# Kernel optimization log

Hardware: AMD Instinct MI355X
Metric: run time of the kernel (lower is better)

The kernel has to match this reference:

```python
import jax, jax.numpy as jnp
import numpy as np

B, S, D, H = 2, 2048, 1024, 16
HD = D // H
MAX_SEQ_LEN = 2048
ROPE_BASE = 10000.0


def _rope(x, pos):
    # x: [B,S,H,HD], pos: [B,S] int positions (already abs+clamped)
    inv_freq = 1.0 / (ROPE_BASE ** (jnp.arange(0, HD, 2, dtype=jnp.float32) / HD))  # [HD/2]
    freqs = pos.astype(jnp.float32)[..., None] * inv_freq  # [B,S,HD/2]
    cos = jnp.cos(freqs)[:, :, None, :]  # [B,S,1,HD/2]
    sin = jnp.sin(freqs)[:, :, None, :]
    x1, x2 = x[..., : HD // 2], x[..., HD // 2 :]
    return jnp.concatenate([x1 * cos - x2 * sin, x2 * cos + x1 * sin], axis=-1)


def setup_inputs() -> dict:
    key = jax.random.key(0)
    ks = jax.random.split(key, 8)
    std = 1.0 / np.sqrt(D)
    x = jax.random.normal(ks[0], (B, S, D), dtype=jnp.float32)
    Wq = jax.random.normal(ks[1], (D, D), dtype=jnp.float32) * std
    Wk = jax.random.normal(ks[2], (D, D), dtype=jnp.float32) * std
    Wv = jax.random.normal(ks[3], (D, D), dtype=jnp.float32) * std
    Wo = jax.random.normal(ks[4], (D, D), dtype=jnp.float32) * std
    bq = jnp.zeros((D,), jnp.float32)
    bk = jnp.zeros((D,), jnp.float32)
    bv = jnp.zeros((D,), jnp.float32)
    bo = jnp.zeros((D,), jnp.float32)
    decay_rate = jnp.float32(0.1)
    # causal mask [B,S,S]
    mask = jnp.broadcast_to(jnp.tril(jnp.ones((S, S), jnp.int32)), (B, S, S))
    # sorted day offsets per batch (monotone time axis)
    days_offset = jnp.sort(jax.random.randint(ks[5], (B, S), 0, MAX_SEQ_LEN), axis=-1).astype(jnp.int32)
    return {"x": x, "Wq": Wq, "bq": bq, "Wk": Wk, "bk": bk, "Wv": Wv, "bv": bv,
            "Wo": Wo, "bo": bo, "decay_rate": decay_rate, "mask": mask, "days_offset": days_offset}


def reference(x, Wq, bq, Wk, bk, Wv, bv, Wo, bo, decay_rate, mask, days_offset):
    b, s, _ = x.shape
    q = (x @ Wq.T + bq).reshape(b, s, H, HD)
    k = (x @ Wk.T + bk).reshape(b, s, H, HD)
    v = (x @ Wv.T + bv).reshape(b, s, H, HD)
    pos = jnp.clip(jnp.abs(days_offset), 0, MAX_SEQ_LEN - 1)
    q = _rope(q, pos)
    k = _rope(k, pos)
    scores = jnp.einsum("bqhd,bkhd->bhqk", q, k) / np.sqrt(HD).astype(np.float32)
    dist = jnp.abs(days_offset[:, :, None] - days_offset[:, None, :]).astype(jnp.float32)  # [B,S,S]
    decay = jnp.exp(-decay_rate * dist)
    scores = scores * decay[:, None, :, :]
    scores = jnp.where(mask[:, None, :, :] == 0, -jnp.inf, scores)
    attn = jax.nn.softmax(scores, axis=-1)
    out = jnp.einsum("bhqk,bkhd->bqhd", attn, v).reshape(b, s, D)
    return out @ Wo.T + bo
```

## Files before the change

kernel.cpp:

```cpp
#include <hip/hip_runtime.h>
#include <hip/hip_bf16.h>


typedef unsigned short u16;
typedef short bf16x8 __attribute__((ext_vector_type(8)));
typedef float f32x4 __attribute__((ext_vector_type(4)));

__device__ __forceinline__ u16 f2bf(float f) {
    unsigned u = __builtin_bit_cast(unsigned, f);
    u += 0x7fffu + ((u >> 16) & 1u);
    return (u16)(u >> 16);
}
__device__ __forceinline__ float bf2f(u16 h) {
    unsigned u = ((unsigned)h) << 16;
    return __builtin_bit_cast(float, u);
}

__global__ __launch_bounds__(256) void convert_all_k(const float* __restrict__ x,
                                                     const float* __restrict__ wq,
                                                     const float* __restrict__ wk,
                                                     const float* __restrict__ wv,
                                                     const float* __restrict__ wo_,
                                                     u16* __restrict__ xb,
                                                     u16* __restrict__ wqkv,
                                                     u16* __restrict__ wob) {
    int i = (blockIdx.x * 256 + threadIdx.x) * 4;
    const float* src;
    u16* dst;
    int off;
    if (i < 4194304) {
        src = x; dst = xb; off = i;
    } else if (i < 5242880) {
        src = wq; dst = wqkv; off = i - 4194304;
    } else if (i < 6291456) {
        src = wk; dst = wqkv + 1048576; off = i - 5242880;
    } else if (i < 7340032) {
        src = wv; dst = wqkv + 2097152; off = i - 6291456;
    } else {
        src = wo_; dst = wob; off = i - 7340032;
    }
    float4 v = *(const float4*)(src + off);
    uint2 o;
    o.x = (unsigned)f2bf(v.x) | ((unsigned)f2bf(v.y) << 16);
    o.y = (unsigned)f2bf(v.z) | ((unsigned)f2bf(v.w) << 16);
    *(uint2*)(dst + off) = o;
}

template <int EPI>
__global__ __launch_bounds__(256) void gemm_bt(const u16* __restrict__ A,
                                               const u16* __restrict__ Bw,
                                               const float* __restrict__ bias0,
                                               const float* __restrict__ bias1,
                                               const float* __restrict__ bias2,
                                               const int* __restrict__ days,
                                               u16* __restrict__ outB,
                                               float* __restrict__ outF,
                                               int M, int N, int K) {
    __shared__ __align__(16) u16 As[2][4096];
    __shared__ __align__(16) u16 Bs[2][4096];
    const int tid = threadIdx.x;
    const int lane = tid & 63;
    const int w = tid >> 6;
    const int wr = w >> 1, wc = w & 1;
    const int lr = lane & 15, lg = lane >> 4;
    const int nbn = N >> 7;
    const int m0 = (blockIdx.x / nbn) << 7;
    const int n0 = (blockIdx.x % nbn) << 7;

    f32x4 acc[4][4] = {};

    const u16* aptr[2];
    const u16* bptr[2];
    int ldsoff[2];
#pragma unroll
    for (int i = 0; i < 2; ++i) {
        int c = (w * 2 + i) * 64 + lane;
        int row = c >> 2, kc = (c & 3) << 3;
        aptr[i] = A + (size_t)(m0 + row) * K + kc;
        bptr[i] = Bw + (size_t)(n0 + row) * K + kc;
        ldsoff[i] = (w * 2 + i) * 512;
    }

#define GSTAGE(K0, BUF)                                                                \
    do {                                                                               \
        _Pragma("unroll") for (int i = 0; i < 2; ++i) {                                \
            __builtin_amdgcn_global_load_lds(                                          \
                (const __attribute__((address_space(1))) void*)(aptr[i] + (K0)),       \
                (__attribute__((address_space(3))) void*)(&As[BUF][ldsoff[i]]), 16, 0, \
                0);                                                                    \
            __builtin_amdgcn_global_load_lds(                                          \
                (const __attribute__((address_space(1))) void*)(bptr[i] + (K0)),       \
                (__attribute__((address_space(3))) void*)(&Bs[BUF][ldsoff[i]]), 16, 0, \
                0);                                                                    \
        }                                                                              \
    } while (0)

    const int nks = K >> 5;
    GSTAGE(0, 0);
    for (int ks = 0; ks < nks; ++ks) {
        const int cur = ks & 1;
        if (ks + 1 < nks) {
            GSTAGE((ks + 1) * 32, cur ^ 1);
            asm volatile("s_waitcnt vmcnt(4)" ::: "memory");
        } else {
            asm volatile("s_waitcnt vmcnt(0)" ::: "memory");
        }
        __builtin_amdgcn_s_barrier();
        bf16x8 af[4], bfr[4];
#pragma unroll
        for (int i = 0; i < 4; ++i)
            af[i] = *(const bf16x8*)(&As[cur][(wr * 64 + i * 16 + lr) * 32 + lg * 8]);
#pragma unroll
        for (int j = 0; j < 4; ++j)
            bfr[j] = *(const bf16x8*)(&Bs[cur][(wc * 64 + j * 16 + lr) * 32 + lg * 8]);
#pragma unroll
        for (int i = 0; i < 4; ++i)
#pragma unroll
            for (int j = 0; j < 4; ++j)
                acc[i][j] = __builtin_amdgcn_mfma_f32_16x16x32_bf16(af[i], bfr[j],
                                                                    acc[i][j], 0, 0, 0);
        __builtin_amdgcn_s_barrier();
    }
#undef GSTAGE

    auto bsel = [&](int ng) -> float {
        if (EPI != 0) return bias0[ng];
        return (ng < 1024) ? bias0[ng] : (ng < 2048) ? bias1[ng - 1024] : bias2[ng - 2048];
    };

    if (EPI == 0 && (n0 + wc * 64) < 2048) {
        const float C1 = -0.41524101186091903f;
        const float inv0 = exp2f((float)lr * C1);
        const float inv1 = exp2f((float)(16 + lr) * C1);
#pragma unroll
        for (int i = 0; i < 4; ++i) {
            int mg = m0 + wr * 64 + i * 16 + lg * 4;
#pragma unroll
            for (int r = 0; r < 4; ++r) {
                int m = mg + r;
                int d = days[m];
                int ad = d < 0 ? -d : d;
                ad = ad > 2047 ? 2047 : ad;
                float pos = (float)ad;
#pragma unroll
                for (int j = 0; j < 2; ++j) {
                    int ng1 = n0 + wc * 64 + j * 16 + lr;
                    int ng2 = ng1 + 32;
                    float x1 = acc[i][j][r] + bsel(ng1);
                    float x2 = acc[i][j + 2][r] + bsel(ng2);
                    float ang = pos * (j ? inv1 : inv0);
                    float sn, cs;
                    __sincosf(ang, &sn, &cs);
                    outB[(size_t)m * N + ng1] = f2bf(x1 * cs - x2 * sn);
                    outB[(size_t)m * N + ng2] = f2bf(x2 * cs + x1 * sn);
                }
            }
        }
    } else {
#pragma unroll
        for (int i = 0; i < 4; ++i) {
            int mg = m0 + wr * 64 + i * 16 + lg * 4;
#pragma unroll
            for (int j = 0; j < 4; ++j) {
                int ng = n0 + wc * 64 + j * 16 + lr;
                float bias = bsel(ng);
#pragma unroll
                for (int r = 0; r < 4; ++r) {
                    float v = acc[i][j][r] + bias;
                    if (EPI == 0)
                        outB[(size_t)(mg + r) * N + ng] = f2bf(v);
                    else
                        outF[(size_t)(mg + r) * N + ng] = v;
                }
            }
        }
    }
}

__global__ __launch_bounds__(256) void v_transpose_k(const u16* __restrict__ qkv,
                                                     u16* __restrict__ vt) {
    __shared__ u16 tile[64][66];
    int st = blockIdx.x & 31;
    int bh = blockIdx.x >> 5;
    int b = bh >> 4, h = bh & 15;
    int s0 = st * 64;
    int t = threadIdx.x;
#pragma unroll
    for (int it = 0; it < 16; ++it) {
        int idx = it * 256 + t;
        int sr = idx >> 6, c = idx & 63;
        tile[sr][c] = qkv[(size_t)(b * 2048 + s0 + sr) * 3072 + 2048 + h * 64 + c];
    }
    __syncthreads();
#pragma unroll
    for (int it = 0; it < 16; ++it) {
        int idx = it * 256 + t;
        int hd = idx >> 6, sc = idx & 63;
        vt[((size_t)(bh * 64 + hd)) * 2048 + s0 + sc] = tile[sc][hd];
    }
}

__global__ __launch_bounds__(256) void vps_k(const u16* __restrict__ vt,
                                             float* __restrict__ vps) {
    __shared__ float ts[32][32];
    const int bh = blockIdx.x >> 1;
    const int d0 = (blockIdx.x & 1) * 32;
    const int dl = threadIdx.x >> 3;
    const int seg = threadIdx.x & 7;
    const u16* vrow = vt + ((size_t)bh * 64 + d0 + dl) * 2048 + seg * 256;
#pragma unroll
    for (int tt = 0; tt < 4; ++tt) {
        float s = 0.f;
#pragma unroll
        for (int i = 0; i < 8; ++i) {
            bf16x8 v = *(const bf16x8*)(vrow + tt * 64 + i * 8);
#pragma unroll
            for (int e = 0; e < 8; ++e) s += bf2f((u16)v[e]);
        }
        ts[dl][seg * 4 + tt] = s;
    }
    __syncthreads();
    if (threadIdx.x < 32) {
        int d = threadIdx.x;
        float acc = 0.f;
        for (int t = 0; t <= 32; ++t) {
            vps[((size_t)bh * 33 + t) * 64 + d0 + d] = acc;
            if (t < 32) acc += ts[d][t];
        }
    }
}


__device__ __forceinline__ void attn_tile(const u16* __restrict__ Ks,
                                          const u16* __restrict__ Vs,
                                          u16* __restrict__ Pw,
                                          const int* __restrict__ dbk,
                                          float dkmax_c, bf16x8 pconst, float pcr,
                                          bf16x8 bq0, bf16x8 bq1, float dq_c, float c1,
                                          int qrel, bool domask,
                                          float& l_part, f32x4* acc, int lr, int lg) {
    if (!domask && __all(dkmax_c - dq_c < -20.0f)) {
        l_part += 16.0f * pcr;
        __builtin_amdgcn_s_setprio(1);
#pragma unroll
        for (int pv = 0; pv < 2; ++pv) {
            int chunk = pv * 4 + lg;
#pragma unroll
            for (int c = 0; c < 4; ++c) {
                const int r3 = c * 16 + lr;
                bf16x8 bv = *(const bf16x8*)(Vs + r3 * 64 + ((chunk ^ (r3 & 7)) << 3));
                acc[c] = __builtin_amdgcn_mfma_f32_16x16x32_bf16(pconst, bv, acc[c], 0, 0, 0);
            }
        }
        __builtin_amdgcn_s_setprio(0);
        return;
    }
    f32x4 st_acc[4];
    __builtin_amdgcn_s_setprio(1);
#pragma unroll
    for (int st = 0; st < 4; ++st) {
        const int r2 = st * 16 + lr;
        const u16* kr = Ks + r2 * 64;
        bf16x8 ka0 = *(const bf16x8*)(kr + ((lg ^ (r2 & 7)) << 3));
        bf16x8 ka1 = *(const bf16x8*)(kr + (((4 + lg) ^ (r2 & 7)) << 3));
        f32x4 t = {};
        t = __builtin_amdgcn_mfma_f32_16x16x32_bf16(ka0, bq0, t, 0, 0, 0);
        t = __builtin_amdgcn_mfma_f32_16x16x32_bf16(ka1, bq1, t, 0, 0, 0);
        st_acc[st] = t;
    }
    __builtin_amdgcn_s_setprio(0);
    const float L2E = 1.4426950408889634f;
    const float POFF = 17.312340490667562f;
    float p[4][4];
#pragma unroll
    for (int st = 0; st < 4; ++st) {
        int4 dk4 = *(const int4*)(dbk + st * 16 + lg * 4);
#pragma unroll
        for (int r = 0; r < 4; ++r) {
            float dkf = (float)((&dk4.x)[r]);
            float dec = exp2f(__builtin_fmaf(dkf, c1, -dq_c));
            float v = st_acc[st][r] * dec;
            p[st][r] = exp2f(__builtin_fmaf(v, L2E, -POFF));
        }
    }
    if (domask) {
#pragma unroll
        for (int st = 0; st < 4; ++st)
#pragma unroll
            for (int r = 0; r < 4; ++r)
                p[st][r] = (st * 16 + lg * 4 + r <= qrel) ? p[st][r] : 0.f;
    }
#pragma unroll
    for (int st = 0; st < 4; ++st)
#pragma unroll
        for (int r = 0; r < 4; ++r) l_part += p[st][r];
#pragma unroll
    for (int st = 0; st < 4; ++st) {
        unsigned lo, hi;
        asm("v_cvt_pk_bf16_f32 %0, %1, %2" : "=v"(lo) : "v"(p[st][0]), "v"(p[st][1]));
        asm("v_cvt_pk_bf16_f32 %0, %1, %2" : "=v"(hi) : "v"(p[st][2]), "v"(p[st][3]));
        uint2 pk;
        pk.x = lo;
        pk.y = hi;
        int chunk = st * 2 + (lg >> 1);
        int idx = lr * 64 + ((chunk ^ (lr & 7)) << 3) + ((lg & 1) << 2);
        *(uint2*)&Pw[idx] = pk;
    }
    __builtin_amdgcn_s_setprio(1);
#pragma unroll
    for (int pv = 0; pv < 2; ++pv) {
        int chunk = pv * 4 + lg;
        bf16x8 pa = *(const bf16x8*)&Pw[lr * 64 + ((chunk ^ (lr & 7)) << 3)];
#pragma unroll
        for (int c = 0; c < 4; ++c) {
            const int r3 = c * 16 + lr;
            bf16x8 bv = *(const bf16x8*)(Vs + r3 * 64 + ((chunk ^ (r3 & 7)) << 3));
            acc[c] = __builtin_amdgcn_mfma_f32_16x16x32_bf16(pa, bv, acc[c], 0, 0, 0);
        }
    }
    __builtin_amdgcn_s_setprio(0);
}

__global__ __launch_bounds__(256, 4) void attn_k(const u16* __restrict__ qkv,
                                                 const u16* __restrict__ vt,
                                                 const int* __restrict__ days,
                                                 const float* __restrict__ decay_p,
                                                 const float* __restrict__ vps,
                                                 u16* __restrict__ attn_out) {
    __shared__ __align__(16) u16 Ks[2][4096];
    __shared__ __align__(16) u16 Vs[2][4096];
    __shared__ __align__(16) u16 Plds[4][1024];
    const int tid = threadIdx.x;
    const int lane = tid & 63;
    const int w = tid >> 6;
    const int lr = lane & 15, lg = lane >> 4;
    const int wg = (blockIdx.x & 7) * 128 + (blockIdx.x >> 3);
    const int qt = wg & 31;
    const int bh = wg >> 5;
    const int b = bh >> 4, h = bh & 15;
    const int qb = qt * 64 + w * 16;
    const float rate = decay_p[0];
    const float c1 = rate * 1.4426950408889634f;

    const u16* qmat = qkv + (size_t)b * 2048 * 3072 + h * 64;
    const u16* kmat = qmat + 1024;
    const u16* vtm = vt + (size_t)bh * 64 * 2048;
    const int* db = days + b * 2048;

    const int cp0 = (w * 2 + 0) * 64 + lane;
    const int cp1 = (w * 2 + 1) * 64 + lane;
    const int r0 = cp0 >> 3, c0 = cp0 & 7;
    const int r1 = cp1 >> 3, c1i = cp1 & 7;
    const u16* ksrc0 = kmat + (size_t)r0 * 3072 + ((c0 ^ (r0 & 7)) << 3);
    const u16* ksrc1 = kmat + (size_t)r1 * 3072 + ((c1i ^ (r1 & 7)) << 3);
    const u16* vsrc0 = vtm + (size_t)r0 * 2048 + ((c0 ^ (r0 & 7)) << 3);
    const u16* vsrc1 = vtm + (size_t)r1 * 2048 + ((c1i ^ (r1 & 7)) << 3);
    const int doff0 = (w * 2 + 0) * 512;
    const int doff1 = (w * 2 + 1) * 512;

#define STAGE(T, SLOT)                                                                 \
    do {                                                                               \
        __builtin_amdgcn_global_load_lds(                                              \
            (const __attribute__((address_space(1))) void*)(ksrc0 +                    \
                                                            (size_t)(T) * 64 * 3072), \
            (__attribute__((address_space(3))) void*)(&Ks[SLOT][doff0]), 16, 0, 0);    \
        __builtin_amdgcn_global_load_lds(                                              \
            (const __attribute__((address_space(1))) void*)(ksrc1 +                    \
                                                            (size_t)(T) * 64 * 3072), \
            (__attribute__((address_space(3))) void*)(&Ks[SLOT][doff1]), 16, 0, 0);    \
        __builtin_amdgcn_global_load_lds(                                              \
            (const __attribute__((address_space(1))) void*)(vsrc0 + (size_t)(T) * 64), \
            (__attribute__((address_space(3))) void*)(&Vs[SLOT][doff0]), 16, 0, 0);    \
        __builtin_amdgcn_global_load_lds(                                              \
            (const __attribute__((address_space(1))) void*)(vsrc1 + (size_t)(T) * 64), \
            (__attribute__((address_space(3))) void*)(&Vs[SLOT][doff1]), 16, 0, 0);    \
    } while (0)

    const float dq00_c = (float)db[qt * 64] * c1 + 3.0f;
    int t0;
    {
        const int l32 = lane & 31;
        float dm = (float)db[l32 * 64 + 63] * c1;
        bool cnd = (lane < qt) && (dm < dq00_c - 20.0f);
        unsigned long long m = __ballot(cnd);
        t0 = (int)__builtin_ctzll(~m);
    }

    STAGE(t0, 0);

    bf16x8 bq0, bq1;
    {
        const u16* qp = qmat + (size_t)(qb + lr) * 3072 + lg * 8;
        bq0 = *(const bf16x8*)qp;
        bq1 = *(const bf16x8*)(qp + 32);
    }
    const float dq_c = (float)db[qb + lr] * c1 + 3.0f;

    const u16 pcu = f2bf(exp2f(-17.312340490667562f));
    const float pcr = bf2f(pcu);
    bf16x8 pconst;
#pragma unroll
    for (int i = 0; i < 8; ++i) pconst[i] = (short)pcu;

    float lp = (float)t0 * 16.0f * pcr;
    f32x4 acc[4];
#pragma unroll
    for (int c = 0; c < 4; ++c) {
        float vv = pcr * vps[((size_t)bh * 33 + t0) * 64 + c * 16 + lr];
        acc[c] = (f32x4){vv, vv, vv, vv};
    }

    for (int kt = t0; kt <= qt; ++kt) {
        const int cur = (kt - t0) & 1;
        if (kt < qt) {
            STAGE(kt + 1, cur ^ 1);
            asm volatile("s_waitcnt vmcnt(4)" ::: "memory");
        } else {
            asm volatile("s_waitcnt vmcnt(0)" ::: "memory");
        }
        __builtin_amdgcn_s_barrier();
        const int* dbk = db + kt * 64;
        const float dkmax_c = (float)dbk[63] * c1;
        attn_tile(Ks[cur], Vs[cur], Plds[w], dbk, dkmax_c, pconst, pcr,
                  bq0, bq1, dq_c, c1, w * 16 + lr, kt == qt, lp, acc, lr, lg);
        __builtin_amdgcn_s_barrier();
    }
#undef STAGE

    float l_full = lp + __shfl_xor(lp, 16);
    l_full += __shfl_xor(l_full, 32);
    float inv_[4];
#pragma unroll
    for (int r = 0; r < 4; ++r) inv_[r] = 1.0f / __shfl(l_full, lg * 4 + r);
#pragma unroll
    for (int c = 0; c < 4; ++c)
#pragma unroll
        for (int r = 0; r < 4; ++r) {
            const int qg = qb + lg * 4 + r;
            attn_out[(size_t)(b * 2048 + qg) * 1024 + h * 64 + c * 16 + lr] =
                f2bf(acc[c][r] * inv_[r]);
        }
}

extern "C" void kernel_launch(void* const* d_in, const int* in_sizes, int n_in,
                              void* d_out, int out_size, void* d_ws, size_t ws_size,
                              hipStream_t stream) {
    const float* x = (const float*)d_in[0];
    const float* Wq = (const float*)d_in[1];
    const float* bq = (const float*)d_in[2];
    const float* Wk = (const float*)d_in[3];
    const float* bk = (const float*)d_in[4];
    const float* Wv = (const float*)d_in[5];
    const float* bv = (const float*)d_in[6];
    const float* Wo = (const float*)d_in[7];
    const float* bo = (const float*)d_in[8];
    const float* decay = (const float*)d_in[9];
    const int* days = (const int*)d_in[11];
    float* out = (float*)d_out;

    char* ws = (char*)d_ws;
    u16* xb = (u16*)(ws);
    u16* wqkv = (u16*)(ws + 8388608);
    u16* wo = (u16*)(ws + 14680064);
    u16* qkvb = (u16*)(ws + 16777216);
    u16* vtb = (u16*)(ws + 41943040);
    u16* attb = (u16*)(ws + 50331648);
    float* vpsb = (float*)(ws + 58720256);

    convert_all_k<<<8192, 256, 0, stream>>>(x, Wq, Wk, Wv, Wo, xb, wqkv, wo);

    gemm_bt<0><<<768, 256, 0, stream>>>(xb, wqkv, bq, bk, bv, days, qkvb, nullptr,
                                        4096, 3072, 1024);
    v_transpose_k<<<1024, 256, 0, stream>>>(qkvb, vtb);
    vps_k<<<64, 256, 0, stream>>>(vtb, vpsb);
    attn_k<<<1024, 256, 0, stream>>>(qkvb, vtb, days, decay, vpsb, attb);
    gemm_bt<1><<<256, 256, 0, stream>>>(attb, wo, bo, nullptr, nullptr, days, nullptr,
                                        out, 4096, 1024, 1024);
}
```

Before: 105.3 us.

## Fuse V transpose into QKV GEMM epilogue and split-K the output projection

The QKV GEMM epilogue now writes V directly in transposed [b,h,hd,s] layout with vectorized 4-element stores. This removes the separate v_transpose kernel and the round trip of V through a 3072-wide buffer, and Q/K are stored with a 2048-wide row stride. The output projection becomes a 512-thread kernel in which two groups of 4 waves each handle half of K, then reduce through LDS. That doubles the waves available for the 256-block launch, at the cost of an extra LDS reduction and extra shared memory.

```diff
diff --git a/kernel.cpp b/kernel.cpp
--- a/kernel.cpp
+++ b/kernel.cpp
@@ -46,16 +46,15 @@
     *(uint2*)(dst + off) = o;
 }
 
-template <int EPI>
-__global__ __launch_bounds__(256) void gemm_bt(const u16* __restrict__ A,
-                                               const u16* __restrict__ Bw,
-                                               const float* __restrict__ bias0,
-                                               const float* __restrict__ bias1,
-                                               const float* __restrict__ bias2,
-                                               const int* __restrict__ days,
-                                               u16* __restrict__ outB,
-                                               float* __restrict__ outF,
-                                               int M, int N, int K) {
+__global__ __launch_bounds__(256) void gemm_qkv(const u16* __restrict__ A,
+                                                const u16* __restrict__ Bw,
+                                                const float* __restrict__ bias0,
+                                                const float* __restrict__ bias1,
+                                                const float* __restrict__ bias2,
+                                                const int* __restrict__ days,
+                                                u16* __restrict__ outB,
+                                                u16* __restrict__ vt,
+                                                int M, int N, int K) {
     __shared__ __align__(16) u16 As[2][4096];
     __shared__ __align__(16) u16 Bs[2][4096];
     const int tid = threadIdx.x;
@@ -124,11 +123,10 @@
 #undef GSTAGE
 
     auto bsel = [&](int ng) -> float {
-        if (EPI != 0) return bias0[ng];
         return (ng < 1024) ? bias0[ng] : (ng < 2048) ? bias1[ng - 1024] : bias2[ng - 2048];
     };
 
-    if (EPI == 0 && (n0 + wc * 64) < 2048) {
+    if ((n0 + wc * 64) < 2048) {
         const float C1 = -0.41524101186091903f;
         const float inv0 = exp2f((float)lr * C1);
         const float inv1 = exp2f((float)(16 + lr) * C1);
@@ -151,52 +149,141 @@
                     float ang = pos * (j ? inv1 : inv0);
                     float sn, cs;
                     __sincosf(ang, &sn, &cs);
-                    outB[(size_t)m * N + ng1] = f2bf(x1 * cs - x2 * sn);
-                    outB[(size_t)m * N + ng2] = f2bf(x2 * cs + x1 * sn);
+                    outB[(size_t)m * 2048 + ng1] = f2bf(x1 * cs - x2 * sn);
+                    outB[(size_t)m * 2048 + ng2] = f2bf(x2 * cs + x1 * sn);
                 }
             }
         }
     } else {
+        const int h = ((n0 + wc * 64) - 2048) >> 6;
 #pragma unroll
         for (int i = 0; i < 4; ++i) {
             int mg = m0 + wr * 64 + i * 16 + lg * 4;
+            int b = mg >> 11, s0 = mg & 2047;
+#pragma unroll
+            for (int j = 0; j < 4; ++j) {
+                int hd = j * 16 + lr;
+                int ng = 2048 + h * 64 + hd;
+                float bias = bsel(ng);
+                ushort4 o;
+                o.x = f2bf(acc[i][j][0] + bias);
+                o.y = f2bf(acc[i][j][1] + bias);
+                o.z = f2bf(acc[i][j][2] + bias);
+                o.w = f2bf(acc[i][j][3] + bias);
+                *(ushort4*)&vt[((size_t)(b * 16 + h) * 64 + hd) * 2048 + s0] = o;
+            }
+        }
+    }
+}
+
+__global__ __launch_bounds__(512, 2) void gemm_out(const u16* __restrict__ A,
+                                                   const u16* __restrict__ Bw,
+                                                   const float* __restrict__ bias0,
+                                                   float* __restrict__ outF,
+                                                   int M, int N, int K) {
+    __shared__ __align__(16) u16 As[2][2][4096];
+    __shared__ __align__(16) u16 Bs[2][2][4096];
+    const int tid = threadIdx.x;
+    const int lane = tid & 63;
+    const int w4 = (tid >> 6) & 3;
+    const int g = tid >> 8;
+    const int wr = w4 >> 1, wc = w4 & 1;
+    const int lr = lane & 15, lg = lane >> 4;
+    const int nbn = N >> 7;
+    const int m0 = (blockIdx.x / nbn) << 7;
+    const int n0 = (blockIdx.x % nbn) << 7;
+    const int kbase = g * (K >> 1);
+
+    f32x4 acc[4][4] = {};
+
+    const u16* aptr[2];
+    const u16* bptr[2];
+    int ldsoff[2];
+#pragma unroll
+    for (int i = 0; i < 2; ++i) {
+        int c = (w4 * 2 + i) * 64 + lane;
+        int row = c >> 2, kc = (c & 3) << 3;
+        aptr[i] = A + (size_t)(m0 + row) * K + kbase + kc;
+        bptr[i] = Bw + (size_t)(n0 + row) * K + kbase + kc;
+        ldsoff[i] = (w4 * 2 + i) * 512;
+    }
+
+#define GSTAGE(K0, BUF)                                                                \
+    do {                                                                               \
+        _Pragma("unroll") for (int i = 0; i < 2; ++i) {                                \
+            __builtin_amdgcn_global_load_lds(                                          \
+                (const __attribute__((address_space(1))) void*)(aptr[i] + (K0)),       \
+                (__attribute__((address_space(3))) void*)(&As[g][BUF][ldsoff[i]]), 16, \
+                0, 0);                                                                 \
+            __builtin_amdgcn_global_load_lds(                                          \
+                (const __attribute__((address_space(1))) void*)(bptr[i] + (K0)),       \
+                (__attribute__((address_space(3))) void*)(&Bs[g][BUF][ldsoff[i]]), 16, \
+                0, 0);                                                                 \
+        }                                                                              \
+    } while (0)
+
+    const int nks = K >> 6;
+    GSTAGE(0, 0);
+    for (int ks = 0; ks < nks; ++ks) {
+        const int cur = ks & 1;
+        if (ks + 1 < nks) {
+            GSTAGE((ks + 1) * 32, cur ^ 1);
+            asm volatile("s_waitcnt vmcnt(4)" ::: "memory");
+        } else {
+            asm volatile("s_waitcnt vmcnt(0)" ::: "memory");
+        }
+        __builtin_amdgcn_s_barrier();
+        bf16x8 af[4], bfr[4];
+#pragma unroll
+        for (int i = 0; i < 4; ++i)
+            af[i] = *(const bf16x8*)(&As[g][cur][(wr * 64 + i * 16 + lr) * 32 + lg * 8]);
+#pragma unroll
+        for (int j = 0; j < 4; ++j)
+            bfr[j] = *(const bf16x8*)(&Bs[g][cur][(wc * 64 + j * 16 + lr) * 32 + lg * 8]);
+#pragma unroll
+        for (int i = 0; i < 4; ++i)
+#pragma unroll
+            for (int j = 0; j < 4; ++j)
+                acc[i][j] = __builtin_amdgcn_mfma_f32_16x16x32_bf16(af[i], bfr[j],
+                                                                    acc[i][j], 0, 0, 0);
+        __builtin_amdgcn_s_barrier();
+    }
+#undef GSTAGE
+
+    float* xch = (float*)&As[0][0][0];
+    const int t256 = tid & 255;
+#pragma unroll
+    for (int hf = 0; hf < 2; ++hf) {
+        __syncthreads();
+        if (g == 1) {
+#pragma unroll
+            for (int i = 0; i < 2; ++i)
+#pragma unroll
+                for (int j = 0; j < 4; ++j)
+                    *(f32x4*)&xch[((t256 * 8) + i * 4 + j) * 4] = acc[hf * 2 + i][j];
+        }
+        __syncthreads();
+        if (g == 0) {
+#pragma unroll
+            for (int i = 0; i < 2; ++i)
+#pragma unroll
+                for (int j = 0; j < 4; ++j)
+                    acc[hf * 2 + i][j] += *(const f32x4*)&xch[((t256 * 8) + i * 4 + j) * 4];
+        }
+    }
+    if (g == 0) {
+#pragma unroll
+        for (int i = 0; i < 4; ++i) {
+            int mg = m0 + wr * 64 + i * 16 + lg * 4;
 #pragma unroll
             for (int j = 0; j < 4; ++j) {
                 int ng = n0 + wc * 64 + j * 16 + lr;
-                float bias = bsel(ng);
-#pragma unroll
-                for (int r = 0; r < 4; ++r) {
-                    float v = acc[i][j][r] + bias;
-                    if (EPI == 0)
-                        outB[(size_t)(mg + r) * N + ng] = f2bf(v);
-                    else
-                        outF[(size_t)(mg + r) * N + ng] = v;
-                }
+                float bias = bias0[ng];
+#pragma unroll
+                for (int r = 0; r < 4; ++r)
+                    outF[(size_t)(mg + r) * N + ng] = acc[i][j][r] + bias;
             }
         }
-    }
-}
-
-__global__ __launch_bounds__(256) void v_transpose_k(const u16* __restrict__ qkv,
-                                                     u16* __restrict__ vt) {
-    __shared__ u16 tile[64][66];
-    int st = blockIdx.x & 31;
-    int bh = blockIdx.x >> 5;
-    int b = bh >> 4, h = bh & 15;
-    int s0 = st * 64;
-    int t = threadIdx.x;
-#pragma unroll
-    for (int it = 0; it < 16; ++it) {
-        int idx = it * 256 + t;
-        int sr = idx >> 6, c = idx & 63;
-        tile[sr][c] = qkv[(size_t)(b * 2048 + s0 + sr) * 3072 + 2048 + h * 64 + c];
-    }
-    __syncthreads();
-#pragma unroll
-    for (int it = 0; it < 16; ++it) {
-        int idx = it * 256 + t;
-        int hd = idx >> 6, sc = idx & 63;
-        vt[((size_t)(bh * 64 + hd)) * 2048 + s0 + sc] = tile[sc][hd];
     }
 }
 
@@ -229,7 +316,6 @@
         }
     }
 }
-
 
 __device__ __forceinline__ void attn_tile(const u16* __restrict__ Ks,
                                           const u16* __restrict__ Vs,
@@ -342,7 +428,7 @@
     const float rate = decay_p[0];
     const float c1 = rate * 1.4426950408889634f;
 
-    const u16* qmat = qkv + (size_t)b * 2048 * 3072 + h * 64;
+    const u16* qmat = qkv + (size_t)b * 2048 * 2048 + h * 64;
     const u16* kmat = qmat + 1024;
     const u16* vtm = vt + (size_t)bh * 64 * 2048;
     const int* db = days + b * 2048;
@@ -351,8 +437,8 @@
     const int cp1 = (w * 2 + 1) * 64 + lane;
     const int r0 = cp0 >> 3, c0 = cp0 & 7;
     const int r1 = cp1 >> 3, c1i = cp1 & 7;
-    const u16* ksrc0 = kmat + (size_t)r0 * 3072 + ((c0 ^ (r0 & 7)) << 3);
-    const u16* ksrc1 = kmat + (size_t)r1 * 3072 + ((c1i ^ (r1 & 7)) << 3);
+    const u16* ksrc0 = kmat + (size_t)r0 * 2048 + ((c0 ^ (r0 & 7)) << 3);
+    const u16* ksrc1 = kmat + (size_t)r1 * 2048 + ((c1i ^ (r1 & 7)) << 3);
     const u16* vsrc0 = vtm + (size_t)r0 * 2048 + ((c0 ^ (r0 & 7)) << 3);
     const u16* vsrc1 = vtm + (size_t)r1 * 2048 + ((c1i ^ (r1 & 7)) << 3);
     const int doff0 = (w * 2 + 0) * 512;
@@ -362,11 +448,11 @@
     do {                                                                               \
         __builtin_amdgcn_global_load_lds(                                              \
             (const __attribute__((address_space(1))) void*)(ksrc0 +                    \
-                                                            (size_t)(T) * 64 * 3072), \
+                                                            (size_t)(T) * 64 * 2048), \
             (__attribute__((address_space(3))) void*)(&Ks[SLOT][doff0]), 16, 0, 0);    \
         __builtin_amdgcn_global_load_lds(                                              \
             (const __attribute__((address_space(1))) void*)(ksrc1 +                    \
-                                                            (size_t)(T) * 64 * 3072), \
+                                                            (size_t)(T) * 64 * 2048), \
             (__attribute__((address_space(3))) void*)(&Ks[SLOT][doff1]), 16, 0, 0);    \
         __builtin_amdgcn_global_load_lds(                                              \
             (const __attribute__((address_space(1))) void*)(vsrc0 + (size_t)(T) * 64), \
@@ -390,7 +476,7 @@
 
     bf16x8 bq0, bq1;
     {
-        const u16* qp = qmat + (size_t)(qb + lr) * 3072 + lg * 8;
+        const u16* qp = qmat + (size_t)(qb + lr) * 2048 + lg * 8;
         bq0 = *(const bf16x8*)qp;
         bq1 = *(const bf16x8*)(qp + 32);
     }
@@ -462,18 +548,16 @@
     u16* xb = (u16*)(ws);
     u16* wqkv = (u16*)(ws + 8388608);
     u16* wo = (u16*)(ws + 14680064);
-    u16* qkvb = (u16*)(ws + 16777216);
+    u16* qkb = (u16*)(ws + 16777216);
     u16* vtb = (u16*)(ws + 41943040);
     u16* attb = (u16*)(ws + 50331648);
     float* vpsb = (float*)(ws + 58720256);
 
     convert_all_k<<<8192, 256, 0, stream>>>(x, Wq, Wk, Wv, Wo, xb, wqkv, wo);
 
-    gemm_bt<0><<<768, 256, 0, stream>>>(xb, wqkv, bq, bk, bv, days, qkvb, nullptr,
-                                        4096, 3072, 1024);
-    v_transpose_k<<<1024, 256, 0, stream>>>(qkvb, vtb);
+    gemm_qkv<<<768, 256, 0, stream>>>(xb, wqkv, bq, bk, bv, days, qkb, vtb, 4096,
+                                      3072, 1024);
     vps_k<<<64, 256, 0, stream>>>(vtb, vpsb);
-    attn_k<<<1024, 256, 0, stream>>>(qkvb, vtb, days, decay, vpsb, attb);
-    gemm_bt<1><<<256, 256, 0, stream>>>(attb, wo, bo, nullptr, nullptr, days, nullptr,
-                                        out, 4096, 1024, 1024);
-}
+    attn_k<<<1024, 256, 0, stream>>>(qkb, vtb, days, decay, vpsb, attb);
+    gemm_out<<<256, 512, 0, stream>>>(attb, wo, bo, out, 4096, 1024, 1024);
+}
```

Measured after the change: 101.5 us. 3.6% less time.
